# Kernel optimization log

Hardware: AMD Instinct MI355X
Metric: run time of the kernel (lower is better)

The kernel has to match this reference:

```python
import jax, jax.numpy as jnp
import numpy as np

TEMPERATURE = 5.0

def setup_inputs() -> dict:
    key = jax.random.key(0)
    k1, k2 = jax.random.split(key)
    B, D = 8192, 128
    features = jax.random.normal(k1, (B, D), dtype=jnp.float32)
    labels = jax.random.randint(k2, (B,), 0, 100, dtype=jnp.int64)
    return {"features": features, "labels": labels, "fac_label": 3}


def reference(features, labels, fac_label):
    # features: [B, D], labels: [B]
    B = features.shape[0]
    # positive-pair mask; note original's mask_scale row-copy loop is a no-op,
    # so mask_scale == mask, and mask_cross_feature == ones (fac_label unused in effect)
    mask = (labels[:, None] == labels[None, :]).astype(features.dtype)  # [B, B]

    sim = jnp.matmul(features, features.T) / TEMPERATURE  # [B, B]
    logits_max = jax.lax.stop_gradient(jnp.max(sim, axis=1, keepdims=True))
    logits = sim - logits_max

    # remove self-contrast (diagonal)
    logits_mask = 1.0 - jnp.eye(B, dtype=features.dtype)
    mask = mask * logits_mask

    exp_logits = jnp.exp(logits) * logits_mask
    log_prob = logits - jnp.log(1e-12 + exp_logits.sum(axis=1, keepdims=True))

    mean_log_prob_pos_mask = (mask * log_prob).sum(axis=1)  # [B]
    # vectorized form of the per-element reciprocal loop: 1/count where count>0 else 0
    cnt = mask.sum(axis=1)
    recip = jnp.where(cnt == 0, 0.0, 1.0 / jnp.where(cnt == 0, 1.0, cnt))

    loss = -(mean_log_prob_pos_mask * recip).mean()
    return loss
```

## Files before the change

### kernel.cpp

```cpp
#include <hip/hip_runtime.h>


#define BN 8192
#define DK 128
#define INV_T 0.2f
#define C1F 0.28853901f
#define C40F 27.7258872f

#define CHUNKS 32
#define CCOLS (BN / CHUNKS)
#define RPB 256
#define RT 4
#define NJT (CCOLS / 16)

#define NCLS 100
#define PB 128
#define PROWS (BN / PB)

#define OFF_FB    0
#define OFF_DIAG  (2 * 1024 * 1024)
#define OFF_PART  (OFF_DIAG + 32768)
#define OFF_GP    (OFF_PART + 2 * 1024 * 1024)
#define OFF_HISTP (OFF_GP + PB * NCLS * DK * 4)
#define OFF_G     (OFF_HISTP + PB * NCLS * 4)
#define OFF_HIST  (OFF_G + NCLS * DK * 4)
#define OFF_BSUM  (OFF_HIST + 512)
#define OFF_CTR   (OFF_BSUM + 128)

typedef __attribute__((ext_vector_type(8))) short bf16x8;
typedef __attribute__((ext_vector_type(4))) float f32x4;

__device__ __forceinline__ unsigned short f2bf(float f) {
    unsigned u = __builtin_bit_cast(unsigned, f);
    u += 0x7fffu + ((u >> 16) & 1u);
    return (unsigned short)(u >> 16);
}

__device__ __forceinline__ float fexp2(float x) {
#if __has_builtin(__builtin_amdgcn_exp2f)
    return __builtin_amdgcn_exp2f(x);
#else
    float r; asm("v_exp_f32 %0, %1" : "=v"(r) : "v"(x)); return r;
#endif
}

__global__ __launch_bounds__(256) void prep_kernel(const float* __restrict__ F,
                                                   const int* __restrict__ labels,
                                                   unsigned short* __restrict__ Fb,
                                                   float* __restrict__ diag,
                                                   float* __restrict__ Gp,
                                                   int* __restrict__ histp,
                                                   unsigned int* __restrict__ ctr) {
    const int t  = threadIdx.x;
    const int b  = blockIdx.x;
    const int r0 = b * PROWS;

    if (b == 0 && t == 0) *ctr = 0u;

    const float4* F4  = (const float4*)F + (size_t)b * (PROWS * DK / 4);
    ushort4*      Fb4 = (ushort4*)Fb + (size_t)b * (PROWS * DK / 4);
#pragma unroll
    for (int k = 0; k < PROWS * DK / 4 / 256; ++k) {
        float4 v = F4[k * 256 + t];
        ushort4 o;
        o.x = f2bf(v.x); o.y = f2bf(v.y); o.z = f2bf(v.z); o.w = f2bf(v.w);
        Fb4[k * 256 + t] = o;
    }

    {
        const int row = r0 + (t >> 2);
        const int q   = t & 3;
        const float4* rp = (const float4*)(F + (size_t)row * DK) + q * 8;
        float s = 0.f;
#pragma unroll
        for (int k = 0; k < 8; ++k) {
            float4 v = rp[k];
            s += v.x * v.x + v.y * v.y + v.z * v.z + v.w * v.w;
        }
        s += __shfl_xor(s, 1);
        s += __shfl_xor(s, 2);
        if (q == 0) diag[row] = s;
    }

    __shared__ int   lh[NCLS];
    __shared__ float gl[NCLS][DK];
    float* glf = (float*)gl;
    if (t < NCLS) lh[t] = 0;
#pragma unroll
    for (int k = 0; k < NCLS * DK / 256; ++k) glf[k * 256 + t] = 0.f;
    __syncthreads();

    if (t < PROWS) atomicAdd(&lh[labels[r0 + t]], 1);

    if (t < DK) {
        for (int rr = 0; rr < PROWS; ++rr) {
            const int row = r0 + rr;
            const int c   = labels[row];
            gl[c][t] += F[(size_t)row * DK + t];
        }
    }
    __syncthreads();

    if (t < NCLS) histp[b * NCLS + t] = lh[t];
#pragma unroll
    for (int k = 0; k < NCLS * DK / 256; ++k) {
        const int idx = k * 256 + t;
        Gp[(size_t)b * (NCLS * DK) + idx] = glf[idx];
    }
}

template <bool DIAGBLK>
__device__ __forceinline__ void supcon_rows(const short* __restrict__ Fb,
                                            float2* __restrict__ part,
                                            int bx, int by) {
    const int t    = threadIdx.x;
    const int wave = t >> 6, lane = t & 63;
    const int quad = lane >> 4, l16 = lane & 15;
    const int rowBase = bx * RPB + wave * (RT * 16);
    const int colBase = by * CCOLS;

    bf16x8 a[RT][4];
#pragma unroll
    for (int rt = 0; rt < RT; ++rt)
#pragma unroll
        for (int kt = 0; kt < 4; ++kt)
            a[rt][kt] = *(const bf16x8*)(Fb + (size_t)(rowBase + rt * 16 + l16) * DK
                                            + kt * 32 + quad * 8);

    float mr[RT][4], Zs[RT][4];
#pragma unroll
    for (int rt = 0; rt < RT; ++rt)
#pragma unroll
        for (int r = 0; r < 4; ++r) { mr[rt][r] = -__builtin_inff(); Zs[rt][r] = 0.f; }

    const short* bp = Fb + (size_t)(colBase + l16) * DK + quad * 8;
    bf16x8 bc[4], bn[4];
#pragma unroll
    for (int kt = 0; kt < 4; ++kt) bc[kt] = *(const bf16x8*)(bp + kt * 32);

    auto STEP = [&](const bf16x8 (&bb)[4], int jtc) {
        const int j0 = colBase + jtc * 16;
#pragma unroll
        for (int rt = 0; rt < RT; ++rt) {
            f32x4 acc = {0.f, 0.f, 0.f, 0.f};
#pragma unroll
            for (int kt = 0; kt < 4; ++kt)
                acc = __builtin_amdgcn_mfma_f32_16x16x32_bf16(a[rt][kt], bb[kt], acc, 0, 0, 0);
            float e[4];
#pragma unroll
            for (int r = 0; r < 4; ++r) {
                const float raw = acc[r];
                mr[rt][r] = fmaxf(mr[rt][r], raw);
                e[r] = fexp2(fmaf(raw, C1F, -40.0f));
            }
            if (DIAGBLK) {
                const int irow0 = rowBase + rt * 16 + quad * 4;
#pragma unroll
                for (int r = 0; r < 4; ++r)
                    if (j0 + l16 == irow0 + r) e[r] = 0.f;
            }
#pragma unroll
            for (int r = 0; r < 4; ++r) Zs[rt][r] += e[r];
        }
    };

    for (int jt = 0; jt < NJT; jt += 2) {
        bp += 16 * DK;
#pragma unroll
        for (int kt = 0; kt < 4; ++kt) bn[kt] = *(const bf16x8*)(bp + kt * 32);
        STEP(bc, jt);
        if (jt + 2 < NJT) {
            bp += 16 * DK;
#pragma unroll
            for (int kt = 0; kt < 4; ++kt) bc[kt] = *(const bf16x8*)(bp + kt * 32);
        }
        STEP(bn, jt + 1);
    }

#pragma unroll
    for (int rt = 0; rt < RT; ++rt)
#pragma unroll
        for (int r = 0; r < 4; ++r) {
            float mm = mr[rt][r], zz = Zs[rt][r];
#pragma unroll
            for (int h = 1; h < 16; h <<= 1) {
                mm = fmaxf(mm, __shfl_xor(mm, h));
                zz += __shfl_xor(zz, h);
            }
            if (l16 == 0)
                part[(size_t)by * BN + rowBase + rt * 16 + quad * 4 + r] =
                    make_float2(mm, zz);
        }
}

__global__ __launch_bounds__(256, 3) void supcon_main(const short* __restrict__ Fb,
                                                      float2* __restrict__ part,
                                                      const float* __restrict__ Gp,
                                                      const int* __restrict__ histp,
                                                      float* __restrict__ G,
                                                      int* __restrict__ hist) {
    if (blockIdx.y == CHUNKS) {
        const int base = blockIdx.x * 256 + threadIdx.x;
        for (int idx = base; idx < NCLS * DK + NCLS; idx += BN) {
            if (idx < NCLS * DK) {
                float s = 0.f;
#pragma unroll 8
                for (int p = 0; p < PB; ++p) s += Gp[(size_t)p * (NCLS * DK) + idx];
                G[idx] = s;
            } else {
                const int c = idx - NCLS * DK;
                int s = 0;
#pragma unroll 8
                for (int p = 0; p < PB; ++p) s += histp[p * NCLS + c];
                hist[c] = s;
            }
        }
        return;
    }
    if (blockIdx.x == blockIdx.y) supcon_rows<true >(Fb, part, blockIdx.x, blockIdx.y);
    else                          supcon_rows<false>(Fb, part, blockIdx.x, blockIdx.y);
}

__global__ __launch_bounds__(256) void supcon_finalize(const float* __restrict__ F,
                                                       const int* __restrict__ labels,
                                                       const float2* __restrict__ part,
                                                       const float* __restrict__ diag,
                                                       const float* __restrict__ G,
                                                       const int* __restrict__ hist,
                                                       float* __restrict__ bsums,
                                                       unsigned int* __restrict__ ctr,
                                                       float* __restrict__ out) {
    const int t = threadIdx.x;
    const int i = blockIdx.x * 256 + t;

    float mraw = -__builtin_inff(), Zm = 0.f;
#pragma unroll 8
    for (int c = 0; c < CHUNKS; ++c) {
        const float2 p = part[(size_t)c * BN + i];
        mraw = fmaxf(mraw, p.x);
        Zm += p.y;
    }
    const int   lbl = labels[i];
    const float cnt = (float)(hist[lbl] - 1);

    const float4* fr = (const float4*)(F + (size_t)i * DK);
    const float4* gr = (const float4*)(G + lbl * DK);
    float dot = 0.f;
#pragma unroll 8
    for (int k = 0; k < DK / 4; ++k) {
        const float4 av = fr[k], gv = gr[k];
        dot += av.x * gv.x + av.y * gv.y + av.z * gv.z + av.w * gv.w;
    }

    const float m = mraw * INV_T;
    const float A = (dot - diag[i]) * INV_T;
    float term = 0.f;
    if (cnt > 0.5f)
        term = (A - cnt * m) / cnt - __logf(1e-12f + Zm * __expf(C40F - m));

    float sum = term;
#pragma unroll
    for (int h = 1; h < 64; h <<= 1) sum += __shfl_xor(sum, h);
    __shared__ float ss[4];
    if ((t & 63) == 0) ss[t >> 6] = sum;
    __syncthreads();
    if (t == 0) {
        bsums[blockIdx.x] = ss[0] + ss[1] + ss[2] + ss[3];
        __threadfence();
        const unsigned old = atomicAdd(ctr, 1u);
        if (old == (BN / 256) - 1) {
            __threadfence();
            float tot = 0.f;
            const volatile float* vb = bsums;
            for (int c = 0; c < BN / 256; ++c) tot += vb[c];
            out[0] = -tot * (1.0f / BN);
        }
    }
}

extern "C" void kernel_launch(void* const* d_in, const int* in_sizes, int n_in,
                              void* d_out, int out_size, void* d_ws, size_t ws_size,
                              hipStream_t stream) {
    const float* F      = (const float*)d_in[0];
    const int*   labels = (const int*)d_in[1];
    float* out = (float*)d_out;
    char*  ws  = (char*)d_ws;

    unsigned short* Fb    = (unsigned short*)(ws + OFF_FB);
    float*          diag  = (float*)(ws + OFF_DIAG);
    float2*         part  = (float2*)(ws + OFF_PART);
    float*          Gp    = (float*)(ws + OFF_GP);
    int*            histp = (int*)(ws + OFF_HISTP);
    float*          G     = (float*)(ws + OFF_G);
    int*            hist  = (int*)(ws + OFF_HIST);
    float*          bsums = (float*)(ws + OFF_BSUM);
    unsigned int*   ctr   = (unsigned int*)(ws + OFF_CTR);

    prep_kernel<<<PB, 256, 0, stream>>>(F, labels, Fb, diag, Gp, histp, ctr);
    supcon_main<<<dim3(BN / RPB, CHUNKS + 1), 256, 0, stream>>>((const short*)Fb, part,
                                                                Gp, histp, G, hist);
    supcon_finalize<<<BN / 256, 256, 0, stream>>>(F, labels, part, diag, G, hist,
                                                  bsums, ctr, out);
}
```

Before: 129.0 us.

## Stage B tiles through swizzled LDS via direct global-to-LDS loads; fuse diag norm into finalize

In the main kernel, each wave used to load its B-column fragments straight from global memory into registers. Now the block cooperatively copies each 16-column tile into double-buffered, XOR-swizzled shared memory using global_load_lds, and all four waves read it from there. This cuts redundant global/L2 traffic because the four waves share each tile, but it adds two block-wide barriers per pair of tiles and drops the occupancy hint from launch bounds. The per-row squared norm is also moved from the prep kernel into finalize, which removes the diag buffer and its pass over the input.

```diff
diff --git a/kernel.cpp b/kernel.cpp
--- a/kernel.cpp
+++ b/kernel.cpp
@@ -18,14 +18,13 @@
 #define PROWS (BN / PB)
 
 #define OFF_FB    0
-#define OFF_DIAG  (2 * 1024 * 1024)
-#define OFF_PART  (OFF_DIAG + 32768)
+#define OFF_PART  (2 * 1024 * 1024)
 #define OFF_GP    (OFF_PART + 2 * 1024 * 1024)
 #define OFF_HISTP (OFF_GP + PB * NCLS * DK * 4)
 #define OFF_G     (OFF_HISTP + PB * NCLS * 4)
 #define OFF_HIST  (OFF_G + NCLS * DK * 4)
 #define OFF_BSUM  (OFF_HIST + 512)
-#define OFF_CTR   (OFF_BSUM + 128)
+#define OFF_CTR   (OFF_BSUM + 256)
 
 typedef __attribute__((ext_vector_type(8))) short bf16x8;
 typedef __attribute__((ext_vector_type(4))) float f32x4;
@@ -44,10 +43,15 @@
 #endif
 }
 
+__device__ __forceinline__ void load_lds16(const void* g, void* l) {
+    __builtin_amdgcn_global_load_lds(
+        (const __attribute__((address_space(1))) unsigned int*)g,
+        (__attribute__((address_space(3))) unsigned int*)l, 16, 0, 0);
+}
+
 __global__ __launch_bounds__(256) void prep_kernel(const float* __restrict__ F,
                                                    const int* __restrict__ labels,
                                                    unsigned short* __restrict__ Fb,
-                                                   float* __restrict__ diag,
                                                    float* __restrict__ Gp,
                                                    int* __restrict__ histp,
                                                    unsigned int* __restrict__ ctr) {
@@ -67,21 +71,6 @@
         Fb4[k * 256 + t] = o;
     }
 
-    {
-        const int row = r0 + (t >> 2);
-        const int q   = t & 3;
-        const float4* rp = (const float4*)(F + (size_t)row * DK) + q * 8;
-        float s = 0.f;
-#pragma unroll
-        for (int k = 0; k < 8; ++k) {
-            float4 v = rp[k];
-            s += v.x * v.x + v.y * v.y + v.z * v.z + v.w * v.w;
-        }
-        s += __shfl_xor(s, 1);
-        s += __shfl_xor(s, 2);
-        if (q == 0) diag[row] = s;
-    }
-
     __shared__ int   lh[NCLS];
     __shared__ float gl[NCLS][DK];
     float* glf = (float*)gl;
@@ -112,7 +101,7 @@
 template <bool DIAGBLK>
 __device__ __forceinline__ void supcon_rows(const short* __restrict__ Fb,
                                             float2* __restrict__ part,
-                                            int bx, int by) {
+                                            int bx, int by, char* smem) {
     const int t    = threadIdx.x;
     const int wave = t >> 6, lane = t & 63;
     const int quad = lane >> 4, l16 = lane & 15;
@@ -133,48 +122,55 @@
 #pragma unroll
         for (int r = 0; r < 4; ++r) { mr[rt][r] = -__builtin_inff(); Zs[rt][r] = 0.f; }
 
-    const short* bp = Fb + (size_t)(colBase + l16) * DK + quad * 8;
-    bf16x8 bc[4], bn[4];
-#pragma unroll
-    for (int kt = 0; kt < 4; ++kt) bc[kt] = *(const bf16x8*)(bp + kt * 32);
-
-    auto STEP = [&](const bf16x8 (&bb)[4], int jtc) {
-        const int j0 = colBase + jtc * 16;
+    const int  L    = wave * 1024 + lane * 16;
+    const int  sw   = (L & ~255) | ((L & 255) ^ ((L >> 4) & 0x70));
+    const char* tile0 = (const char*)(Fb + (size_t)colBase * DK);
+    char*       dst0  = smem + wave * 1024;
+
+    int roff[4];
+#pragma unroll
+    for (int kt = 0; kt < 4; ++kt)
+        roff[kt] = l16 * 256 + ((kt * 64 + quad * 16) ^ ((l16 & 7) << 4));
+
+    auto STAGE = [&](int bufoff, int jt) {
+        load_lds16(tile0 + (size_t)jt * 4096 + sw, dst0 + bufoff);
+    };
+
+    auto COMPUTE = [&](int bufoff, int jt) {
+        bf16x8 bb[4];
+#pragma unroll
+        for (int kt = 0; kt < 4; ++kt)
+            bb[kt] = *(const bf16x8*)(smem + bufoff + roff[kt]);
+        const int j0 = colBase + jt * 16;
 #pragma unroll
         for (int rt = 0; rt < RT; ++rt) {
             f32x4 acc = {0.f, 0.f, 0.f, 0.f};
 #pragma unroll
             for (int kt = 0; kt < 4; ++kt)
                 acc = __builtin_amdgcn_mfma_f32_16x16x32_bf16(a[rt][kt], bb[kt], acc, 0, 0, 0);
-            float e[4];
 #pragma unroll
             for (int r = 0; r < 4; ++r) {
                 const float raw = acc[r];
                 mr[rt][r] = fmaxf(mr[rt][r], raw);
-                e[r] = fexp2(fmaf(raw, C1F, -40.0f));
+                float e = fexp2(fmaf(raw, C1F, -40.0f));
+                if (DIAGBLK) {
+                    const int irow0 = rowBase + rt * 16 + quad * 4;
+                    if (j0 + l16 == irow0 + r) e = 0.f;
+                }
+                Zs[rt][r] += e;
             }
-            if (DIAGBLK) {
-                const int irow0 = rowBase + rt * 16 + quad * 4;
-#pragma unroll
-                for (int r = 0; r < 4; ++r)
-                    if (j0 + l16 == irow0 + r) e[r] = 0.f;
-            }
-#pragma unroll
-            for (int r = 0; r < 4; ++r) Zs[rt][r] += e[r];
         }
     };
 
+    STAGE(0, 0);
+    __syncthreads();
     for (int jt = 0; jt < NJT; jt += 2) {
-        bp += 16 * DK;
-#pragma unroll
-        for (int kt = 0; kt < 4; ++kt) bn[kt] = *(const bf16x8*)(bp + kt * 32);
-        STEP(bc, jt);
-        if (jt + 2 < NJT) {
-            bp += 16 * DK;
-#pragma unroll
-            for (int kt = 0; kt < 4; ++kt) bc[kt] = *(const bf16x8*)(bp + kt * 32);
-        }
-        STEP(bn, jt + 1);
+        STAGE(4096, jt + 1);
+        COMPUTE(0, jt);
+        __syncthreads();
+        if (jt + 2 < NJT) STAGE(0, jt + 2);
+        COMPUTE(4096, jt + 1);
+        __syncthreads();
     }
 
 #pragma unroll
@@ -193,12 +189,13 @@
         }
 }
 
-__global__ __launch_bounds__(256, 3) void supcon_main(const short* __restrict__ Fb,
-                                                      float2* __restrict__ part,
-                                                      const float* __restrict__ Gp,
-                                                      const int* __restrict__ histp,
-                                                      float* __restrict__ G,
-                                                      int* __restrict__ hist) {
+__global__ __launch_bounds__(256) void supcon_main(const short* __restrict__ Fb,
+                                                   float2* __restrict__ part,
+                                                   const float* __restrict__ Gp,
+                                                   const int* __restrict__ histp,
+                                                   float* __restrict__ G,
+                                                   int* __restrict__ hist) {
+    __shared__ alignas(16) char smem[8192];
     if (blockIdx.y == CHUNKS) {
         const int base = blockIdx.x * 256 + threadIdx.x;
         for (int idx = base; idx < NCLS * DK + NCLS; idx += BN) {
@@ -217,14 +214,13 @@
         }
         return;
     }
-    if (blockIdx.x == blockIdx.y) supcon_rows<true >(Fb, part, blockIdx.x, blockIdx.y);
-    else                          supcon_rows<false>(Fb, part, blockIdx.x, blockIdx.y);
+    if (blockIdx.x == blockIdx.y) supcon_rows<true >(Fb, part, blockIdx.x, blockIdx.y, smem);
+    else                          supcon_rows<false>(Fb, part, blockIdx.x, blockIdx.y, smem);
 }
 
 __global__ __launch_bounds__(256) void supcon_finalize(const float* __restrict__ F,
                                                        const int* __restrict__ labels,
                                                        const float2* __restrict__ part,
-                                                       const float* __restrict__ diag,
                                                        const float* __restrict__ G,
                                                        const int* __restrict__ hist,
                                                        float* __restrict__ bsums,
@@ -245,15 +241,16 @@
 
     const float4* fr = (const float4*)(F + (size_t)i * DK);
     const float4* gr = (const float4*)(G + lbl * DK);
-    float dot = 0.f;
+    float dot = 0.f, nrm = 0.f;
 #pragma unroll 8
     for (int k = 0; k < DK / 4; ++k) {
         const float4 av = fr[k], gv = gr[k];
         dot += av.x * gv.x + av.y * gv.y + av.z * gv.z + av.w * gv.w;
+        nrm += av.x * av.x + av.y * av.y + av.z * av.z + av.w * av.w;
     }
 
     const float m = mraw * INV_T;
-    const float A = (dot - diag[i]) * INV_T;
+    const float A = (dot - nrm) * INV_T;
     float term = 0.f;
     if (cnt > 0.5f)
         term = (A - cnt * m) / cnt - __logf(1e-12f + Zm * __expf(C40F - m));
@@ -287,7 +284,6 @@
     char*  ws  = (char*)d_ws;
 
     unsigned short* Fb    = (unsigned short*)(ws + OFF_FB);
-    float*          diag  = (float*)(ws + OFF_DIAG);
     float2*         part  = (float2*)(ws + OFF_PART);
     float*          Gp    = (float*)(ws + OFF_GP);
     int*            histp = (int*)(ws + OFF_HISTP);
@@ -296,9 +292,9 @@
     float*          bsums = (float*)(ws + OFF_BSUM);
     unsigned int*   ctr   = (unsigned int*)(ws + OFF_CTR);
 
-    prep_kernel<<<PB, 256, 0, stream>>>(F, labels, Fb, diag, Gp, histp, ctr);
+    prep_kernel<<<PB, 256, 0, stream>>>(F, labels, Fb, Gp, histp, ctr);
     supcon_main<<<dim3(BN / RPB, CHUNKS + 1), 256, 0, stream>>>((const short*)Fb, part,
                                                                 Gp, histp, G, hist);
-    supcon_finalize<<<BN / 256, 256, 0, stream>>>(F, labels, part, diag, G, hist,
+    supcon_finalize<<<BN / 256, 256, 0, stream>>>(F, labels, part, G, hist,
                                                   bsums, ctr, out);
 }
```

After: 116.7 us. 9.5% less time.
